# Kernel optimization log

Measured on AMD Instinct MI355X. Metric: run time of the kernel, lower is better.

Reference implementation:

```python
import jax, jax.numpy as jnp
import numpy as np

PHI = 1.6180339887498949  # golden ratio, matches torch PHI constant

B, S, V, D, N, L = 128, 64, 1024, 512, 1024, 2


def setup_inputs() -> dict:
    key = jax.random.key(0)
    ks = jax.random.split(key, 8)
    input_ids = jax.random.randint(ks[0], (B, S), 0, V)
    # nn.Embedding(V, 2D), std=0.02 then *0.5
    token_embedding = jax.random.normal(ks[1], (V, 2 * D), dtype=jnp.float32) * 0.01
    # per-layer resonant params, stacked over L layers
    layers_W = jax.random.normal(ks[2], (L, N, D), dtype=jnp.float32) * 0.02
    layers_bias = jnp.zeros((L, N), dtype=jnp.float32)
    layers_proj_real = jax.random.normal(ks[3], (L, D, N), dtype=jnp.float32) * 0.02
    layers_proj_imag = jax.random.normal(ks[4], (L, D, N), dtype=jnp.float32) * 0.02
    output_proj = jax.random.normal(ks[5], (V, D), dtype=jnp.float32) * 0.02
    return {
        "input_ids": input_ids,
        "token_embedding": token_embedding,
        "layers_W": layers_W,
        "layers_bias": layers_bias,
        "layers_proj_real": layers_proj_real,
        "layers_proj_imag": layers_proj_imag,
        "output_proj": output_proj,
    }


def _rin_forward(input_ids, token_embedding, layers_W, layers_bias,
                 layers_proj_real, layers_proj_imag, output_proj):
    b, s = input_ids.shape
    d = token_embedding.shape[1] // 2
    emb = token_embedding[input_ids]            # (b, s, 2d) gather
    w_emb = jnp.swapaxes(emb[:, :, :d], 0, 1)   # (s, b, d)
    b_emb = jnp.swapaxes(emb[:, :, d:], 0, 1)   # (s, b, d)
    t_vals = jnp.arange(s, dtype=jnp.float32) * PHI  # (s,)
    n_layers = layers_W.shape[0]

    def step(carry, inp):
        h_real, h_imag = carry
        w_t, b_t, t_val = inp
        wavelength = 1.0 + jnp.abs(w_t)                       # (b, d)
        theta_r = h_real / wavelength + b_t + t_val
        theta_i = h_imag / wavelength + b_t + t_val
        sr, cr = jnp.sin(theta_r), jnp.cos(theta_r)
        si, ci = jnp.sin(theta_i), jnp.cos(theta_i)
        # complex rotation: (cr + i sr) * (ci + i si)
        h_real = cr * ci - sr * si
        h_imag = cr * si + sr * ci
        h = h_real + h_imag
        for l in range(n_layers):  # small fixed layer count
            theta = h @ layers_W[l].T + layers_bias[l] + t_val      # (b, N)
            out = jnp.cos(theta) @ layers_proj_real[l].T + jnp.sin(theta) @ layers_proj_imag[l].T
            h = h + jax.nn.silu(out)
        return (h_real, h_imag), h

    h0 = jnp.zeros((b, d), dtype=jnp.float32)
    _, hs = jax.lax.scan(step, (h0, h0), (w_emb, b_emb, t_vals))
    return hs[-1] @ output_proj.T  # (b, vocab)


def reference(input_ids, token_embedding, layers_W, layers_bias,
              layers_proj_real, layers_proj_imag, output_proj):
    return _rin_forward(input_ids, token_embedding, layers_W, layers_bias,
                        layers_proj_real, layers_proj_imag, output_proj)
```

## Files before the change

### kernel.cpp

```cpp
#include <hip/hip_runtime.h>
#include <hip/hip_bf16.h>
#include <cmath>

#define PHI_F   1.6180339887498949f
#define INV2PI  0.15915494309189535f
#define SQRT2F  1.41421356237309505f
#define TLASTF  (63.0f * 1.6180339887498949f)
#define LOG2EF  1.4426950408889634f

typedef __attribute__((ext_vector_type(8))) short bf16x8;
typedef __attribute__((ext_vector_type(4))) float f32x4;

__device__ __forceinline__ unsigned short bf16rn(float x) {
    const unsigned u = __float_as_uint(x);
    return (unsigned short)((u + 0x7fffu + ((u >> 16) & 1u)) >> 16);
}

__device__ __forceinline__ bf16x8 cvt8(float4 a, float4 b) {
    union { bf16x8 v; __hip_bfloat162 h2[4]; } u;
    u.h2[0] = __float22bfloat162_rn(make_float2(a.x, a.y));
    u.h2[1] = __float22bfloat162_rn(make_float2(a.z, a.w));
    u.h2[2] = __float22bfloat162_rn(make_float2(b.x, b.y));
    u.h2[3] = __float22bfloat162_rn(make_float2(b.z, b.w));
    return u.v;
}

__global__ __launch_bounds__(256) void rinrec_k(
    const int* __restrict__ ids, const float* __restrict__ te,
    float* __restrict__ h, unsigned short* __restrict__ hh)
{
    const int b = blockIdx.x >> 1;
    const int d = ((blockIdx.x & 1) << 8) + threadIdx.x;
    __shared__ int sid[64];
    if (threadIdx.x < 64) sid[threadIdx.x] = ids[b * 64 + threadIdx.x];
    __syncthreads();

    float wv[2][8], bev[2][8];
    #pragma unroll
    for (int j = 0; j < 8; ++j) {
        const int id = sid[j];
        wv[0][j]  = te[id * 1024 + d];
        bev[0][j] = te[id * 1024 + 512 + d];
    }
    float v = 0.f;
    #pragma unroll
    for (int g = 0; g < 8; ++g) {
        const int cur = g & 1, nxt = cur ^ 1;
        if (g < 7) {
            #pragma unroll
            for (int j = 0; j < 8; ++j) {
                const int id = sid[(g + 1) * 8 + j];
                wv[nxt][j]  = te[id * 1024 + d];
                bev[nxt][j] = te[id * 1024 + 512 + d];
            }
        }
        #pragma unroll
        for (int j = 0; j < 8; ++j) {
            const int t = g * 8 + j;
            const float rlam = __builtin_amdgcn_rcpf(1.0f + fabsf(wv[cur][j]));
            const float a2 = (SQRT2F * INV2PI) * rlam;
            const float b2 = fmaf(2.0f * INV2PI, bev[cur][j],
                                  fmaf((float)t, 2.0f * PHI_F * INV2PI, 0.125f));
            v = __builtin_amdgcn_sinf(__builtin_amdgcn_fractf(fmaf(v, a2, b2)));
        }
    }
    const float u = SQRT2F * v;
    h[b * 512 + d] = u;
    hh[b * 512 + d] = bf16rn(u);
}

template<int KC>
__device__ __forceinline__ f32x4 frag1(
    const unsigned short* __restrict__ Ah, const float* __restrict__ B,
    int lda, int ldb, int m0, int n0, int k0, int lane)
{
    const int rr = lane & 15;
    const int ko = (lane >> 4) * 8;
    const unsigned short* ap = Ah + (size_t)(m0 + rr) * lda + k0 + ko;
    const float*          bp = B  + (size_t)(n0 + rr) * ldb + k0 + ko;
    f32x4 acc = {0.f, 0.f, 0.f, 0.f};
    #pragma unroll
    for (int kk = 0; kk < KC; kk += 32) {
        const bf16x8 ah = *(const bf16x8*)(ap + kk);
        const float4 b0 = *(const float4*)(bp + kk);
        const float4 b1 = *(const float4*)(bp + kk + 4);
        acc = __builtin_amdgcn_mfma_f32_16x16x32_bf16(ah, cvt8(b0, b1), acc, 0, 0, 0);
    }
    return acc;
}

__global__ __launch_bounds__(512) void theta_k(
    const unsigned short* __restrict__ hh,
    const float* __restrict__ W, const float* __restrict__ bias,
    unsigned short* __restrict__ ct, unsigned short* __restrict__ st)
{
    __shared__ float red[8][260];
    const int lane = threadIdx.x & 63;
    const int w = threadIdx.x >> 6;
    const int nt = blockIdx.x & 63, mt = blockIdx.x >> 6;
    const f32x4 acc = frag1<64>(hh, W, 512, 512,
                                mt * 16, nt * 16, w * 64, lane);
    *(f32x4*)&red[w][lane * 4] = acc;
    __syncthreads();
    if (w < 2) {
        float4 s = {0.f, 0.f, 0.f, 0.f};
        #pragma unroll
        for (int ww = 0; ww < 8; ++ww) {
            const float4 q = *(const float4*)&red[ww][lane * 4];
            s.x += q.x; s.y += q.y; s.z += q.z; s.w += q.w;
        }
        unsigned short* dst = w ? st : ct;
        const int col = lane & 15, rb = (lane >> 4) * 4;
        const int n = nt * 16 + col;
        const float bn = bias[n] + TLASTF;
        const float sv[4] = {s.x, s.y, s.z, s.w};
        #pragma unroll
        for (int r = 0; r < 4; ++r) {
            const int m = mt * 16 + rb + r;
            const float fr = __builtin_amdgcn_fractf((sv[r] + bn) * INV2PI);
            const float vv = w ? __builtin_amdgcn_sinf(fr)
                               : __builtin_amdgcn_cosf(fr);
            dst[m * 1024 + n] = bf16rn(vv);
        }
    }
}

__global__ __launch_bounds__(1024) void pv_k(
    const unsigned short* __restrict__ ct, const unsigned short* __restrict__ st,
    const float* __restrict__ Pr, const float* __restrict__ Pi,
    float* __restrict__ h, unsigned short* __restrict__ hh)
{
    __shared__ float red[16][260];
    const int lane = threadIdx.x & 63;
    const int w = threadIdx.x >> 6;
    const int nt = blockIdx.x & 31, mt = blockIdx.x >> 5;
    const int p = w >> 3, k0 = (w & 7) * 128;
    const unsigned short* A = p ? st : ct;
    const float* B = p ? Pi : Pr;
    const f32x4 acc = frag1<128>(A, B, 1024, 1024,
                                 mt * 16, nt * 16, k0, lane);
    *(f32x4*)&red[w][lane * 4] = acc;
    __syncthreads();
    if (w == 0) {
        float4 s = {0.f, 0.f, 0.f, 0.f};
        #pragma unroll
        for (int ww = 0; ww < 16; ++ww) {
            const float4 q = *(const float4*)&red[ww][lane * 4];
            s.x += q.x; s.y += q.y; s.z += q.z; s.w += q.w;
        }
        const int col = lane & 15, rb = (lane >> 4) * 4;
        const int dn = nt * 16 + col;
        const float sv[4] = {s.x, s.y, s.z, s.w};
        #pragma unroll
        for (int r = 0; r < 4; ++r) {
            const int m = mt * 16 + rb + r;
            const float x = sv[r];
            const float sig = __builtin_amdgcn_rcpf(
                1.0f + __builtin_amdgcn_exp2f(-LOG2EF * x));
            const float val = h[m * 512 + dn] + x * sig;
            h[m * 512 + dn] = val;
            hh[m * 512 + dn] = bf16rn(val);
        }
    }
}

__global__ __launch_bounds__(512) void logits_k(
    const unsigned short* __restrict__ hh,
    const float* __restrict__ op, float* __restrict__ out)
{
    __shared__ float red[8][260];
    const int lane = threadIdx.x & 63;
    const int w = threadIdx.x >> 6;
    const int nt = blockIdx.x & 63, mt = blockIdx.x >> 6;
    const f32x4 acc = frag1<64>(hh, op, 512, 512,
                                mt * 16, nt * 16, w * 64, lane);
    *(f32x4*)&red[w][lane * 4] = acc;
    __syncthreads();
    if (w == 0) {
        float4 s = {0.f, 0.f, 0.f, 0.f};
        #pragma unroll
        for (int ww = 0; ww < 8; ++ww) {
            const float4 q = *(const float4*)&red[ww][lane * 4];
            s.x += q.x; s.y += q.y; s.z += q.z; s.w += q.w;
        }
        const int col = lane & 15, rb = (lane >> 4) * 4;
        const int n = nt * 16 + col;
        const float sv[4] = {s.x, s.y, s.z, s.w};
        #pragma unroll
        for (int r = 0; r < 4; ++r)
            out[(size_t)(mt * 16 + rb + r) * 1024 + n] = sv[r];
    }
}

extern "C" void kernel_launch(void* const* d_in, const int* in_sizes, int n_in,
                              void* d_out, int out_size, void* d_ws, size_t ws_size,
                              hipStream_t stream) {
    const int*   ids   = (const int*)d_in[0];
    const float* te    = (const float*)d_in[1];
    const float* W     = (const float*)d_in[2];
    const float* bias  = (const float*)d_in[3];
    const float* Pr    = (const float*)d_in[4];
    const float* Pi    = (const float*)d_in[5];
    const float* oproj = (const float*)d_in[6];
    float* out = (float*)d_out;

    float*          h  = (float*)d_ws;
    unsigned short* hh = (unsigned short*)(h + 65536);
    unsigned short* ct = hh + 65536;
    unsigned short* st = ct + 131072;

    rinrec_k<<<256, 256, 0, stream>>>(ids, te, h, hh);

    for (int l = 0; l < 2; ++l) {
        theta_k<<<512, 512, 0, stream>>>(
            hh, W + (size_t)l * 524288, bias + l * 1024, ct, st);
        pv_k<<<256, 1024, 0, stream>>>(
            ct, st, Pr + (size_t)l * 524288, Pi + (size_t)l * 524288, h, hh);
    }

    logits_k<<<512, 512, 0, stream>>>(hh, oproj, out);
}
```

Measured before the change: 42.37 us.

## Prefetch weight matrices into cache during recurrence and pack two tiles per block

The recurrence kernel now runs 128 blocks of 512 threads (one batch row each) and adds 128 extra blocks that read all W, Pr, Pi and output_proj weights and throw the values away. This warms the L2/MALL caches while the latency-bound recurrence runs, so the later GEMM kernels hit cache instead of HBM. theta_k and logits_k also now pack two 16x16 output tiles into each 1024-thread block, halving the block count. The warm-up adds extra bandwidth use, and it depends on the cache being able to hold about 14 MB of weights.

```diff
diff --git a/kernel.cpp b/kernel.cpp
--- a/kernel.cpp
+++ b/kernel.cpp
@@ -25,16 +25,41 @@
     return u.v;
 }
 
-__global__ __launch_bounds__(256) void rinrec_k(
+__global__ __launch_bounds__(512) void rec_warm_k(
     const int* __restrict__ ids, const float* __restrict__ te,
+    const float* __restrict__ W, const float* __restrict__ Pr,
+    const float* __restrict__ Pi, const float* __restrict__ op,
     float* __restrict__ h, unsigned short* __restrict__ hh)
 {
-    const int b = blockIdx.x >> 1;
-    const int d = ((blockIdx.x & 1) << 8) + threadIdx.x;
+    const int bid = blockIdx.x, tid = threadIdx.x;
+    if (bid >= 128) {
+        const int g = (bid - 128) * 512 + tid;
+        const float4* Wf  = (const float4*)W;
+        const float4* Prf = (const float4*)Pr;
+        const float4* Pif = (const float4*)Pi;
+        const float4* opf = (const float4*)op;
+        float4 a = {0.f, 0.f, 0.f, 0.f};
+        #pragma unroll
+        for (int i = 0; i < 4; ++i) {
+            const float4 v0 = Wf[g + i * 65536];
+            const float4 v1 = Prf[g + i * 65536];
+            const float4 v2 = Pif[g + i * 65536];
+            a.x += v0.x + v1.x + v2.x; a.y += v0.y + v1.y + v2.y;
+            a.z += v0.z + v1.z + v2.z; a.w += v0.w + v1.w + v2.w;
+        }
+        #pragma unroll
+        for (int i = 0; i < 2; ++i) {
+            const float4 v = opf[g + i * 65536];
+            a.x += v.x; a.y += v.y; a.z += v.z; a.w += v.w;
+        }
+        const float s = a.x + a.y + a.z + a.w;
+        asm volatile("" :: "v"(s));
+        return;
+    }
     __shared__ int sid[64];
-    if (threadIdx.x < 64) sid[threadIdx.x] = ids[b * 64 + threadIdx.x];
-    __syncthreads();
-
+    if (tid < 64) sid[tid] = ids[bid * 64 + tid];
+    __syncthreads();
+    const int d = tid;
     float wv[2][8], bev[2][8];
     #pragma unroll
     for (int j = 0; j < 8; ++j) {
@@ -65,8 +90,8 @@
         }
     }
     const float u = SQRT2F * v;
-    h[b * 512 + d] = u;
-    hh[b * 512 + d] = bf16rn(u);
+    h[bid * 512 + d] = u;
+    hh[bid * 512 + d] = bf16rn(u);
 }
 
 template<int KC>
@@ -89,27 +114,30 @@
     return acc;
 }
 
-__global__ __launch_bounds__(512) void theta_k(
+__global__ __launch_bounds__(1024) void theta_k(
     const unsigned short* __restrict__ hh,
     const float* __restrict__ W, const float* __restrict__ bias,
     unsigned short* __restrict__ ct, unsigned short* __restrict__ st)
 {
-    __shared__ float red[8][260];
+    __shared__ float red[16][260];
     const int lane = threadIdx.x & 63;
     const int w = threadIdx.x >> 6;
-    const int nt = blockIdx.x & 63, mt = blockIdx.x >> 6;
+    const int tile = blockIdx.x * 2 + (w >> 3);
+    const int nt = tile & 63, mt = tile >> 6;
     const f32x4 acc = frag1<64>(hh, W, 512, 512,
-                                mt * 16, nt * 16, w * 64, lane);
+                                mt * 16, nt * 16, (w & 7) * 64, lane);
     *(f32x4*)&red[w][lane * 4] = acc;
     __syncthreads();
-    if (w < 2) {
+    if ((w & 7) < 2) {
+        const int grp = (w >> 3) * 8;
         float4 s = {0.f, 0.f, 0.f, 0.f};
         #pragma unroll
         for (int ww = 0; ww < 8; ++ww) {
-            const float4 q = *(const float4*)&red[ww][lane * 4];
+            const float4 q = *(const float4*)&red[grp + ww][lane * 4];
             s.x += q.x; s.y += q.y; s.z += q.z; s.w += q.w;
         }
-        unsigned short* dst = w ? st : ct;
+        const int sel = w & 7;
+        unsigned short* dst = sel ? st : ct;
         const int col = lane & 15, rb = (lane >> 4) * 4;
         const int n = nt * 16 + col;
         const float bn = bias[n] + TLASTF;
@@ -118,8 +146,8 @@
         for (int r = 0; r < 4; ++r) {
             const int m = mt * 16 + rb + r;
             const float fr = __builtin_amdgcn_fractf((sv[r] + bn) * INV2PI);
-            const float vv = w ? __builtin_amdgcn_sinf(fr)
-                               : __builtin_amdgcn_cosf(fr);
+            const float vv = sel ? __builtin_amdgcn_sinf(fr)
+                                 : __builtin_amdgcn_cosf(fr);
             dst[m * 1024 + n] = bf16rn(vv);
         }
     }
@@ -164,23 +192,25 @@
     }
 }
 
-__global__ __launch_bounds__(512) void logits_k(
+__global__ __launch_bounds__(1024) void logits_k(
     const unsigned short* __restrict__ hh,
     const float* __restrict__ op, float* __restrict__ out)
 {
-    __shared__ float red[8][260];
+    __shared__ float red[16][260];
     const int lane = threadIdx.x & 63;
     const int w = threadIdx.x >> 6;
-    const int nt = blockIdx.x & 63, mt = blockIdx.x >> 6;
+    const int tile = blockIdx.x * 2 + (w >> 3);
+    const int nt = tile & 63, mt = tile >> 6;
     const f32x4 acc = frag1<64>(hh, op, 512, 512,
-                                mt * 16, nt * 16, w * 64, lane);
+                                mt * 16, nt * 16, (w & 7) * 64, lane);
     *(f32x4*)&red[w][lane * 4] = acc;
     __syncthreads();
-    if (w == 0) {
+    if ((w & 7) == 0) {
+        const int grp = (w >> 3) * 8;
         float4 s = {0.f, 0.f, 0.f, 0.f};
         #pragma unroll
         for (int ww = 0; ww < 8; ++ww) {
-            const float4 q = *(const float4*)&red[ww][lane * 4];
+            const float4 q = *(const float4*)&red[grp + ww][lane * 4];
             s.x += q.x; s.y += q.y; s.z += q.z; s.w += q.w;
         }
         const int col = lane & 15, rb = (lane >> 4) * 4;
@@ -209,14 +239,14 @@
     unsigned short* ct = hh + 65536;
     unsigned short* st = ct + 131072;
 
-    rinrec_k<<<256, 256, 0, stream>>>(ids, te, h, hh);
+    rec_warm_k<<<256, 512, 0, stream>>>(ids, te, W, Pr, Pi, oproj, h, hh);
 
     for (int l = 0; l < 2; ++l) {
-        theta_k<<<512, 512, 0, stream>>>(
+        theta_k<<<256, 1024, 0, stream>>>(
             hh, W + (size_t)l * 524288, bias + l * 1024, ct, st);
         pv_k<<<256, 1024, 0, stream>>>(
             ct, st, Pr + (size_t)l * 524288, Pi + (size_t)l * 524288, h, hh);
     }
 
-    logits_k<<<512, 512, 0, stream>>>(hh, oproj, out);
-}
+    logits_k<<<256, 1024, 0, stream>>>(hh, oproj, out);
+}
```

Result: slower. 43.35 us (+2.3%).
